# Kernel tuning notes

Hardware: AMD Instinct MI355X
Metric: run time of the kernel (lower is better)

The kernel has to match this reference:

```python
import jax, jax.numpy as jnp
import numpy as np

B, T, E, V, L = 8, 128, 256, 8192, 5  # batch, block_size, embedding_size (== num heads, head_size=1), vocab, num blocks


def setup_inputs() -> dict:
    key = jax.random.key(0)
    ks = jax.random.split(key, 12)
    s = 0.02
    return {
        "idxs": jax.random.randint(ks[0], (B, T), 0, V),
        "targets": jax.random.randint(ks[1], (B, T), 0, V),
        "emb": jax.random.normal(ks[2], (V, E)) * s,
        "pos_emb": jax.random.normal(ks[3], (T, E)) * s,
        "Wq": jax.random.normal(ks[4], (L, E, E)) * s,  # per-layer: E heads, each Linear(E,1); columns are heads
        "Wk": jax.random.normal(ks[5], (L, E, E)) * s,
        "Wv": jax.random.normal(ks[6], (L, E, E)) * s,
        "Wfc": jax.random.normal(ks[7], (L, E, E)) * s,
        "bfc": jnp.zeros((L, E)),
        "Wlm": jax.random.normal(ks[8], (E, V)) * s,
        "blm": jnp.zeros((V,)),
    }


def _block(x, Wq, Wk, Wv, Wfc, bfc):
    # E heads of head_size=1: projecting with [E,E] gives [B,T,H] with H==E,
    # column h being head h's scalar q/k/v. Faithful to per-head Linear(E,1).
    q = x @ Wq
    k = x @ Wk
    v = x @ Wv
    scores = jnp.einsum('bih,bjh->bhij', q, k)  # no 1/sqrt(d) scaling (faithful)
    i = jnp.arange(x.shape[1])
    causal = i[:, None] >= i[None, :]  # masked_fill where tril==0, i.e. j>i -> -inf
    scores = jnp.where(causal[None, None], scores, -jnp.inf)
    attn = jax.nn.softmax(scores, axis=-2)  # NOTE: source softmaxes over dim=-2 (query axis) -- faithful quirk
    out = jnp.einsum('bhij,bjh->bih', attn, v)  # concat of heads == H axis order
    x = x + out
    return x + jax.nn.relu(x @ Wfc + bfc)


def reference(idxs, targets, emb, pos_emb, Wq, Wk, Wv, Wfc, bfc, Wlm, blm):
    x = emb[idxs] + pos_emb[: idxs.shape[1]]  # [B,T,E]
    for l in range(L):
        x = _block(x, Wq[l], Wk[l], Wv[l], Wfc[l], bfc[l])
    logits = (x @ Wlm + blm).reshape(-1, V)  # [B*T, V], as source views before CE
    logp = jax.nn.log_softmax(logits, axis=-1)
    loss = -jnp.take_along_axis(logp, targets.reshape(-1, 1), axis=-1).mean()
    return logits, loss
```

## Files before the change

### kernel.cpp

```cpp
#include <hip/hip_runtime.h>

#define BB 8
#define TT 128
#define EE 256
#define VV 8192
#define LL 5
#define NROWS (BB*TT)

typedef __attribute__((ext_vector_type(8))) short bf16x8;
typedef __attribute__((ext_vector_type(4))) float f32x4;

__device__ inline ushort f2bf(float f) {
    union { float f; unsigned u; } c; c.f = f;
    unsigned u = c.u;
    return (ushort)((u + 0x7FFF + ((u >> 16) & 1)) >> 16);
}

__device__ __forceinline__ void gload_lds16(const void* g, void* l) {
    __builtin_amdgcn_global_load_lds((const __attribute__((address_space(1))) unsigned int*)g,
                                     (__attribute__((address_space(3))) unsigned int*)l,
                                     16, 0, 0);
}


__global__ __launch_bounds__(256) void prep_kernel(
        const int* __restrict__ idxs, const float* __restrict__ emb, const float* __restrict__ pos,
        const float* __restrict__ Wq, const float* __restrict__ Wk,
        const float* __restrict__ Wv, const float* __restrict__ Wfc,
        const float* __restrict__ Wlm,
        float* __restrict__ x0, ushort* __restrict__ WTs, ushort* __restrict__ WlmT,
        float* __restrict__ loss_cell) {
    int id = blockIdx.x;
    if (id == 0) {
        if (threadIdx.x == 0) *loss_cell = 0.f;
        return;
    }
    if (id < 513) {
        __shared__ ushort ts[64][72];
        int idw = id - 1;
        int v0 = (idw & 127) * 64, k0 = (idw >> 7) * 64;
        int lane = threadIdx.x & 63, w = threadIdx.x >> 6;
        for (int kk = w; kk < 64; kk += 4)
            ts[lane][kk] = f2bf(Wlm[(size_t)(k0 + kk)*VV + v0 + lane]);
        __syncthreads();
        for (int vv = w; vv < 64; vv += 4) {
            int r = v0 + vv, k = k0 + lane;
            WlmT[(size_t)r*256 + (k & 128) + ((k & 127) ^ ((r & 7) << 3))] = ts[vv][lane];
        }
        return;
    }
    if (id < 833) {
        __shared__ ushort ts[64][72];
        int idm = id - 513;
        int mat = idm >> 4, tile = idm & 15;
        int l = mat >> 2, type = mat & 3;
        const float* src = (type == 0 ? Wq : type == 1 ? Wk : type == 2 ? Wv : Wfc) + l*EE*EE;
        ushort* dst = WTs + mat*EE*EE;
        int i0 = (tile >> 2) * 64, o0 = (tile & 3) * 64;
        int lane = threadIdx.x & 63, w = threadIdx.x >> 6;
        for (int ii = w; ii < 64; ii += 4)
            ts[lane][ii] = f2bf(src[(i0 + ii)*EE + o0 + lane]);
        __syncthreads();
        for (int oo = w; oo < 64; oo += 4) {
            int r = o0 + oo, k = i0 + lane;
            dst[(size_t)r*256 + (k & 128) + ((k & 127) ^ ((r & 7) << 3))] = ts[oo][lane];
        }
        return;
    }
    int h = threadIdx.x;
    int row0 = (id - 833) * 4;
    for (int r = 0; r < 4; ++r) {
        int row = row0 + r;
        x0[row*EE + h] = emb[(size_t)idxs[row]*EE + h] + pos[(row & (TT-1))*EE + h];
    }
}

__global__ __launch_bounds__(512, 4) void qkv_attn_kernel(
        float* __restrict__ x, const ushort* __restrict__ WTl) {
    __shared__ __align__(16) ushort Xs[128*128];
    __shared__ __align__(16) ushort Bs[32*128];
    __shared__ float QS[8*132], KS[8*132], VS[8*132], MS[8*132], RV[8*132];
    int tid = threadIdx.x, lane = tid & 63, w = tid >> 6;
    int b  = blockIdx.x >> 5;
    int h0 = (blockIdx.x & 31) * 8;

    f32x4 acc[2] = {};
    int rband = w*16 + (lane & 15);
    int kq = (lane >> 4) * 8;

    #pragma unroll
    for (int half = 0; half < 2; ++half) {
        if (half) __syncthreads();
        {
            int rsub = lane >> 5, cb = (lane & 31) * 4;
            for (int rr2 = w*2; rr2 < 128; rr2 += 16) {
                int rr = rr2 + rsub;
                float4 v = *(const float4*)&x[(size_t)(b*TT + rr)*EE + half*128 + cb];
                ushort4 hh; hh.x = f2bf(v.x); hh.y = f2bf(v.y); hh.z = f2bf(v.z); hh.w = f2bf(v.w);
                *(ushort4*)&Xs[rr*128 + (cb ^ ((rr & 7) << 3))] = hh;
            }
        }
        {
            int rowg = w*4 + (lane >> 4);
            int rowv = rowg < 24 ? rowg : 23;
            int mat = rowv >> 3, col = h0 + (rowv & 7);
            const ushort* src = WTl + (size_t)mat*EE*EE + (size_t)col*256
                              + half*128 + (lane & 15)*8;
            gload_lds16(src, &Bs[w*4*128]);
        }
        __syncthreads();
        for (int ks = 0; ks < 4; ++ks) {
            int kk = ks*32 + kq;
            bf16x8 a = *(const bf16x8*)&Xs[rband*128 + (kk ^ ((rband & 7) << 3))];
            #pragma unroll
            for (int ct = 0; ct < 2; ++ct) {
                int c = ct*16 + (lane & 15);
                bf16x8 bb = *(const bf16x8*)&Bs[c*128 + (kk ^ ((c & 7) << 3))];
                acc[ct] = __builtin_amdgcn_mfma_f32_16x16x32_bf16(a, bb, acc[ct], 0, 0, 0);
            }
        }
    }
    {
        int r_ = w*16 + ((lane >> 4) << 2);
        #pragma unroll
        for (int ct = 0; ct < 2; ++ct) {
            int col24 = ct*16 + (lane & 15);
            #pragma unroll
            for (int j = 0; j < 4; ++j) {
                float val = acc[ct][j];
                int row = r_ + j;
                if (col24 < 8)       QS[col24*132 + row] = val;
                else if (col24 < 16) KS[(col24-8)*132 + row] = val;
                else if (col24 < 24) VS[(col24-16)*132 + row] = val;
            }
        }
    }
    __syncthreads();

    int g = w, lg = lane;
    {
        int j0 = lg*2;
        float k0 = KS[g*132 + j0], k1 = KS[g*132 + j0 + 1];
        float q0j = QS[g*132 + j0], q1j = QS[g*132 + j0 + 1];
        float pmax = fmaxf(q0j, q1j), pmin = fminf(q0j, q1j);
        #pragma unroll
        for (int d = 1; d < 64; d <<= 1) {
            float om = __shfl_down(pmax, d);
            float on = __shfl_down(pmin, d);
            if (lg + d < 64) { pmax = fmaxf(pmax, om); pmin = fminf(pmin, on); }
        }
        float nx = __shfl_down(pmax, 1), nn = __shfl_down(pmin, 1);
        float sp1 = (lg == 63) ? q1j : fmaxf(q1j, nx);
        float sn1 = (lg == 63) ? q1j : fminf(q1j, nn);
        float m0 = (k0 >= 0.f) ? k0*pmax : k0*pmin;
        float m1 = (k1 >= 0.f) ? k1*sp1  : k1*sn1;
        float z0 = 0.f, z1 = 0.f;
        for (int i = j0; i < TT; ++i) {
            float qi = QS[g*132 + i];
            z0 += __expf(qi*k0 - m0);
            z1 += (i >= j0+1) ? __expf(qi*k1 - m1) : 0.f;
        }
        MS[g*132 + j0]     = m0;
        MS[g*132 + j0 + 1] = m1;
        RV[g*132 + j0]     = VS[g*132 + j0] / z0;
        RV[g*132 + j0 + 1] = VS[g*132 + j0 + 1] / z1;
    }
    __syncthreads();
    float a0 = 0.f, a1 = 0.f;
    {
        int i0 = lg*2;
        float q0 = QS[g*132 + i0], q1 = QS[g*132 + i0 + 1];
        for (int j = 0; j <= i0 + 1; ++j) {
            float kj = KS[g*132 + j], mj = MS[g*132 + j], rj = RV[g*132 + j];
            float e0 = __expf(q0*kj - mj) * rj;
            float e1 = __expf(q1*kj - mj) * rj;
            a0 += (j <= i0) ? e0 : 0.f;
            a1 += e1;
        }
    }
    __syncthreads();
    VS[g*132 + lg*2]     = a0;
    VS[g*132 + lg*2 + 1] = a1;
    __syncthreads();

    {
        int row = tid >> 2, cp = (tid & 3) * 2;
        size_t gx = (size_t)(b*TT + row)*EE + h0 + cp;
        float2 xv = *(float2*)&x[gx];
        xv.x += VS[cp*132 + row];
        xv.y += VS[(cp+1)*132 + row];
        *(float2*)&x[gx] = xv;
    }
}

__global__ __launch_bounds__(256, 4) void fc_mfma(
        const float* __restrict__ xin, const ushort* __restrict__ WT,
        const float* __restrict__ bfc, float* __restrict__ xout) {
    __shared__ __align__(16) ushort As[64*128];
    __shared__ __align__(16) ushort Bs[64*128];
    int tid = threadIdx.x, lane = tid & 63, w = tid >> 6;
    int c0 = blockIdx.x * 64;
    int r0 = blockIdx.y * 64;

    f32x4 acc[4] = {};
    int rband = w*16 + (lane & 15);
    int kq = (lane >> 4) * 8;

    #pragma unroll
    for (int half = 0; half < 2; ++half) {
        if (half) __syncthreads();
        {
            int rsub = lane >> 5, cb = (lane & 31) * 4;
            for (int rr2 = w*2; rr2 < 64; rr2 += 8) {
                int rr = rr2 + rsub;
                float4 v = *(const float4*)&xin[(size_t)(r0 + rr)*EE + half*128 + cb];
                ushort4 hh; hh.x = f2bf(v.x); hh.y = f2bf(v.y); hh.z = f2bf(v.z); hh.w = f2bf(v.w);
                *(ushort4*)&As[rr*128 + (cb ^ ((rr & 7) << 3))] = hh;
            }
        }
        for (int rg = w*4; rg < 64; rg += 16) {
            int row = c0 + rg + (lane >> 4);
            const ushort* src = WT + (size_t)row*256 + half*128 + (lane & 15)*8;
            gload_lds16(src, &Bs[rg*128]);
        }
        __syncthreads();
        for (int ks = 0; ks < 4; ++ks) {
            int kk = ks*32 + kq;
            bf16x8 a = *(const bf16x8*)&As[rband*128 + (kk ^ ((rband & 7) << 3))];
            #pragma unroll
            for (int n = 0; n < 4; ++n) {
                int c = n*16 + (lane & 15);
                bf16x8 b = *(const bf16x8*)&Bs[c*128 + (kk ^ ((c & 7) << 3))];
                acc[n] = __builtin_amdgcn_mfma_f32_16x16x32_bf16(a, b, acc[n], 0, 0, 0);
            }
        }
    }
    int grow0 = r0 + w*16 + ((lane >> 4) << 2);
    #pragma unroll
    for (int n = 0; n < 4; ++n) {
        int col = c0 + n*16 + (lane & 15);
        float bias = bfc[col];
        #pragma unroll
        for (int j = 0; j < 4; ++j) {
            size_t idx = (size_t)(grow0 + j)*EE + col;
            xout[idx] = xin[idx] + fmaxf(acc[n][j] + bias, 0.f);
        }
    }
}

__global__ __launch_bounds__(512, 4) void lm_mfma_kernel(
        const float* __restrict__ x, const ushort* __restrict__ WlmT,
        const float* __restrict__ blm, float* __restrict__ out,
        float* __restrict__ pm, float* __restrict__ pz) {
    __shared__ __align__(16) char LDSb[128*132*4];
    ushort* As = (ushort*)LDSb;
    ushort* Bs = (ushort*)LDSb + 128*128;
    float*  fst = (float*)LDSb;
    int tid = threadIdx.x;
    int lane = tid & 63, w = tid >> 6;
    int c0 = blockIdx.x * 128;
    int r0 = blockIdx.y * 128;

    int wr = (w >> 2) * 64, wc = (w & 3) * 32;
    f32x4 acc[4][2] = {};
    int kq = (lane >> 4) * 8;

    #pragma unroll
    for (int half = 0; half < 2; ++half) {
        if (half) __syncthreads();
        {
            int rsub = lane >> 5, cb = (lane & 31) * 4;
            for (int rr2 = w*2; rr2 < 128; rr2 += 16) {
                int rr = rr2 + rsub;
                float4 v = *(const float4*)&x[(size_t)(r0 + rr)*EE + half*128 + cb];
                ushort4 hh; hh.x = f2bf(v.x); hh.y = f2bf(v.y); hh.z = f2bf(v.z); hh.w = f2bf(v.w);
                *(ushort4*)&As[rr*128 + (cb ^ ((rr & 7) << 3))] = hh;
            }
        }
        for (int rg = w*4; rg < 128; rg += 32) {
            int row = c0 + rg + (lane >> 4);
            const ushort* src = WlmT + (size_t)row*256 + half*128 + (lane & 15)*8;
            gload_lds16(src, &Bs[rg*128]);
        }
        __syncthreads();
        for (int ks = 0; ks < 4; ++ks) {
            int kk = ks*32 + kq;
            bf16x8 a[4], bfr[2];
            #pragma unroll
            for (int m = 0; m < 4; ++m) {
                int rband = wr + m*16 + (lane & 15);
                a[m] = *(const bf16x8*)&As[rband*128 + (kk ^ ((rband & 7) << 3))];
            }
            #pragma unroll
            for (int n = 0; n < 2; ++n) {
                int c = wc + n*16 + (lane & 15);
                bfr[n] = *(const bf16x8*)&Bs[c*128 + (kk ^ ((c & 7) << 3))];
            }
            #pragma unroll
            for (int m = 0; m < 4; ++m)
                #pragma unroll
                for (int n = 0; n < 2; ++n)
                    acc[m][n] = __builtin_amdgcn_mfma_f32_16x16x32_bf16(a[m], bfr[n], acc[m][n], 0, 0, 0);
        }
    }
    __syncthreads();

    float bias[2];
    #pragma unroll
    for (int n = 0; n < 2; ++n) bias[n] = blm[c0 + wc + n*16 + (lane & 15)];
    #pragma unroll
    for (int m = 0; m < 4; ++m) {
        int rw = wr + m*16 + (lane >> 4)*4;
        #pragma unroll
        for (int j = 0; j < 4; ++j) {
            int row = rw + j;
            float vals[2];
            float vmax = -INFINITY;
            #pragma unroll
            for (int n = 0; n < 2; ++n) {
                vals[n] = acc[m][n][j] + bias[n];
                fst[row*132 + wc + n*16 + (lane & 15)] = vals[n];
                vmax = fmaxf(vmax, vals[n]);
            }
            #pragma unroll
            for (int msk = 1; msk <= 8; msk <<= 1) vmax = fmaxf(vmax, __shfl_xor(vmax, msk));
            float z = 0.f;
            #pragma unroll
            for (int n = 0; n < 2; ++n) z += __expf(vals[n] - vmax);
            #pragma unroll
            for (int msk = 1; msk <= 8; msk <<= 1) z += __shfl_xor(z, msk);
            if ((lane & 15) == 0) {
                pm[(size_t)(r0 + row)*256 + blockIdx.x*4 + (w & 3)] = vmax;
                pz[(size_t)(r0 + row)*256 + blockIdx.x*4 + (w & 3)] = z;
            }
        }
    }
    __syncthreads();
    #pragma unroll
    for (int it = 0; it < 8; ++it) {
        int k = tid + it*512;
        int row = k >> 5, c4 = (k & 31)*4;
        float4 v = *(float4*)&fst[row*132 + c4];
        *(float4*)&out[(size_t)(r0 + row)*VV + c0 + c4] = v;
    }
}

__global__ void loss_kernel(const float* __restrict__ pm, const float* __restrict__ pz,
                            const float* __restrict__ logits, const int* __restrict__ targets,
                            float* __restrict__ out_last) {
    int r = blockIdx.x;
    int t = threadIdx.x;
    __shared__ float sm[256], sz[256];
    float m = pm[(size_t)r*256 + t];
    float z = pz[(size_t)r*256 + t];
    sm[t] = m; __syncthreads();
    for (int s = 128; s > 0; s >>= 1) {
        if (t < s) sm[t] = fmaxf(sm[t], sm[t + s]);
        __syncthreads();
    }
    float M = sm[0];
    sz[t] = z * __expf(m - M); __syncthreads();
    for (int s = 128; s > 0; s >>= 1) {
        if (t < s) sz[t] += sz[t + s];
        __syncthreads();
    }
    if (t == 0) {
        float lse = M + logf(sz[0]);
        atomicAdd(out_last, (lse - logits[(size_t)r*VV + targets[r]]) * (1.0f / NROWS));
    }
}

extern "C" void kernel_launch(void* const* d_in, const int* in_sizes, int n_in,
                              void* d_out, int out_size, void* d_ws, size_t ws_size,
                              hipStream_t stream) {
    const int*   idxs    = (const int*)d_in[0];
    const int*   targets = (const int*)d_in[1];
    const float* emb     = (const float*)d_in[2];
    const float* pos     = (const float*)d_in[3];
    const float* Wq      = (const float*)d_in[4];
    const float* Wk      = (const float*)d_in[5];
    const float* Wv      = (const float*)d_in[6];
    const float* Wfc     = (const float*)d_in[7];
    const float* bfc     = (const float*)d_in[8];
    const float* Wlm     = (const float*)d_in[9];
    const float* blm     = (const float*)d_in[10];
    float* out = (float*)d_out;
    float* loss_cell = out + (size_t)NROWS * VV;

    float* ws = (float*)d_ws;
    float*  xa   = ws;
    float*  xb   = xa + NROWS*EE;
    float*  pm   = xb + NROWS*EE;
    float*  pz   = pm + NROWS*256;
    ushort* WTs  = (ushort*)(pz + NROWS*256);
    ushort* WlmT = WTs + 20*EE*EE;

    prep_kernel<<<1089, 256, 0, stream>>>(idxs, emb, pos, Wq, Wk, Wv, Wfc, Wlm,
                                          xa, WTs, WlmT, loss_cell);

    for (int l = 0; l < LL; ++l) {
        float* xi = (l & 1) ? xb : xa;
        float* xo = (l & 1) ? xa : xb;
        qkv_attn_kernel<<<256, 512, 0, stream>>>(xi, WTs + (size_t)l*4*EE*EE);
        fc_mfma<<<dim3(4, 16), 256, 0, stream>>>(xi, WTs + (size_t)(l*4 + 3)*EE*EE,
                                                 bfc + l*EE, xo);
    }

    lm_mfma_kernel<<<dim3(VV/128, NROWS/128), 512, 0, stream>>>(xb, WlmT, blm, out, pm, pz);
    loss_kernel<<<NROWS, 256, 0, stream>>>(pm, pz, out, targets, loss_cell);
}
```

Measured before the change: 204.2 us.

## Fuse previous layer's FC into next layer's QKV-attention kernel

```diff
diff --git a/kernel.cpp b/kernel.cpp
--- a/kernel.cpp
+++ b/kernel.cpp
@@ -15,6 +15,10 @@
     unsigned u = c.u;
     return (ushort)((u + 0x7FFF + ((u >> 16) & 1)) >> 16);
 }
+__device__ inline float bf2f(ushort u) {
+    union { unsigned u; float f; } c; c.u = ((unsigned)u) << 16;
+    return c.f;
+}
 
 __device__ __forceinline__ void gload_lds16(const void* g, void* l) {
     __builtin_amdgcn_global_load_lds((const __attribute__((address_space(1))) unsigned int*)g,
@@ -24,11 +28,10 @@
 
 
 __global__ __launch_bounds__(256) void prep_kernel(
-        const int* __restrict__ idxs, const float* __restrict__ emb, const float* __restrict__ pos,
         const float* __restrict__ Wq, const float* __restrict__ Wk,
         const float* __restrict__ Wv, const float* __restrict__ Wfc,
         const float* __restrict__ Wlm,
-        float* __restrict__ x0, ushort* __restrict__ WTs, ushort* __restrict__ WlmT,
+        ushort* __restrict__ WTs, ushort* __restrict__ WlmT,
         float* __restrict__ loss_cell) {
     int id = blockIdx.x;
     if (id == 0) {
@@ -49,7 +52,7 @@
         }
         return;
     }
-    if (id < 833) {
+    {
         __shared__ ushort ts[64][72];
         int idm = id - 513;
         int mat = idm >> 4, tile = idm & 15;
@@ -65,61 +68,127 @@
             int r = o0 + oo, k = i0 + lane;
             dst[(size_t)r*256 + (k & 128) + ((k & 127) ^ ((r & 7) << 3))] = ts[oo][lane];
         }
-        return;
-    }
-    int h = threadIdx.x;
-    int row0 = (id - 833) * 4;
-    for (int r = 0; r < 4; ++r) {
-        int row = row0 + r;
-        x0[row*EE + h] = emb[(size_t)idxs[row]*EE + h] + pos[(row & (TT-1))*EE + h];
-    }
-}
-
-__global__ __launch_bounds__(512, 4) void qkv_attn_kernel(
-        float* __restrict__ x, const ushort* __restrict__ WTl) {
-    __shared__ __align__(16) ushort Xs[128*128];
-    __shared__ __align__(16) ushort Bs[32*128];
-    __shared__ float QS[8*132], KS[8*132], VS[8*132], MS[8*132], RV[8*132];
+    }
+}
+
+template<bool FIRST>
+__global__ __launch_bounds__(512, 2) void layer_kernel(
+        const float* __restrict__ y_in, float* __restrict__ y_out,
+        const ushort* __restrict__ WTfc, const float* __restrict__ bfc_prev,
+        const ushort* __restrict__ WTqkv,
+        const int* __restrict__ idxs, const float* __restrict__ emb,
+        const float* __restrict__ pos) {
+    __shared__ __align__(16) ushort Zbuf[128*256];
+    __shared__ __align__(16) char U[49152];
+    __shared__ __align__(16) ushort Bsq[32*128];
+    ushort* Ybuf = (ushort*)U;
+    ushort* BsF  = (ushort*)U + 128*128;
+    float* QS = (float*)U;
+    float* KS = QS + 8*132;
+    float* VS = KS + 8*132;
+    float* MS = VS + 8*132;
+    float* RV = MS + 8*132;
     int tid = threadIdx.x, lane = tid & 63, w = tid >> 6;
     int b  = blockIdx.x >> 5;
     int h0 = (blockIdx.x & 31) * 8;
 
+    if (FIRST) {
+        for (int rr = w; rr < 128; rr += 8) {
+            int id = idxs[b*TT + rr];
+            float4 v = *(const float4*)&emb[(size_t)id*EE + lane*4];
+            float4 p = *(const float4*)&pos[rr*EE + lane*4];
+            ushort4 hh;
+            hh.x = f2bf(v.x + p.x); hh.y = f2bf(v.y + p.y);
+            hh.z = f2bf(v.z + p.z); hh.w = f2bf(v.w + p.w);
+            int k0 = lane*4;
+            *(ushort4*)&Zbuf[rr*256 + (k0 & 128) + ((k0 & 127) ^ ((rr & 7) << 3))] = hh;
+        }
+    } else {
+        f32x4 accz[4][4] = {};
+        int rband = w*16 + (lane & 15);
+        int kq = (lane >> 4) * 8;
+        #pragma unroll
+        for (int half = 0; half < 2; ++half) {
+            __syncthreads();
+            {
+                int rsub = lane >> 5, cb = (lane & 31) * 4;
+                for (int rr2 = w*2; rr2 < 128; rr2 += 16) {
+                    int rr = rr2 + rsub;
+                    float4 v = *(const float4*)&y_in[(size_t)(b*TT + rr)*EE + half*128 + cb];
+                    ushort4 hh;
+                    hh.x = f2bf(v.x); hh.y = f2bf(v.y); hh.z = f2bf(v.z); hh.w = f2bf(v.w);
+                    *(ushort4*)&Ybuf[rr*128 + (cb ^ ((rr & 7) << 3))] = hh;
+                }
+            }
+            #pragma unroll
+            for (int cg = 0; cg < 4; ++cg) {
+                __syncthreads();
+                {
+                    int rg = w*4 + (lane >> 4);
+                    const ushort* s0 = WTfc + (size_t)(cg*64 + rg)*256 + half*128 + (lane & 15)*8;
+                    gload_lds16(s0, &BsF[(size_t)w*4*128]);
+                    const ushort* s1 = WTfc + (size_t)(cg*64 + 32 + rg)*256 + half*128 + (lane & 15)*8;
+                    gload_lds16(s1, &BsF[(size_t)(32 + w*4)*128]);
+                }
+                __syncthreads();
+                for (int ks = 0; ks < 4; ++ks) {
+                    int kk = ks*32 + kq;
+                    bf16x8 a = *(const bf16x8*)&Ybuf[rband*128 + (kk ^ ((rband & 7) << 3))];
+                    #pragma unroll
+                    for (int n = 0; n < 4; ++n) {
+                        int c = n*16 + (lane & 15);
+                        bf16x8 bb = *(const bf16x8*)&BsF[c*128 + (kk ^ ((c & 7) << 3))];
+                        accz[cg][n] = __builtin_amdgcn_mfma_f32_16x16x32_bf16(a, bb, accz[cg][n], 0, 0, 0);
+                    }
+                }
+            }
+        }
+        __syncthreads();
+        int grow0 = w*16 + ((lane >> 4) << 2);
+        #pragma unroll
+        for (int cg = 0; cg < 4; ++cg) {
+            #pragma unroll
+            for (int n = 0; n < 4; ++n) {
+                int col = cg*64 + n*16 + (lane & 15);
+                float bias = bfc_prev[col];
+                #pragma unroll
+                for (int j = 0; j < 4; ++j) {
+                    int row = grow0 + j;
+                    float yv = y_in[(size_t)(b*TT + row)*EE + col];
+                    float z = yv + fmaxf(accz[cg][n][j] + bias, 0.f);
+                    Zbuf[row*256 + (col & 128) + ((col & 127) ^ ((row & 7) << 3))] = f2bf(z);
+                }
+            }
+        }
+    }
+
     f32x4 acc[2] = {};
     int rband = w*16 + (lane & 15);
     int kq = (lane >> 4) * 8;
-
     #pragma unroll
     for (int half = 0; half < 2; ++half) {
-        if (half) __syncthreads();
-        {
-            int rsub = lane >> 5, cb = (lane & 31) * 4;
-            for (int rr2 = w*2; rr2 < 128; rr2 += 16) {
-                int rr = rr2 + rsub;
-                float4 v = *(const float4*)&x[(size_t)(b*TT + rr)*EE + half*128 + cb];
-                ushort4 hh; hh.x = f2bf(v.x); hh.y = f2bf(v.y); hh.z = f2bf(v.z); hh.w = f2bf(v.w);
-                *(ushort4*)&Xs[rr*128 + (cb ^ ((rr & 7) << 3))] = hh;
-            }
-        }
+        __syncthreads();
         {
             int rowg = w*4 + (lane >> 4);
             int rowv = rowg < 24 ? rowg : 23;
             int mat = rowv >> 3, col = h0 + (rowv & 7);
-            const ushort* src = WTl + (size_t)mat*EE*EE + (size_t)col*256
+            const ushort* src = WTqkv + (size_t)mat*EE*EE + (size_t)col*256
                               + half*128 + (lane & 15)*8;
-            gload_lds16(src, &Bs[w*4*128]);
+            gload_lds16(src, &Bsq[(size_t)w*4*128]);
         }
         __syncthreads();
         for (int ks = 0; ks < 4; ++ks) {
             int kk = ks*32 + kq;
-            bf16x8 a = *(const bf16x8*)&Xs[rband*128 + (kk ^ ((rband & 7) << 3))];
+            bf16x8 a = *(const bf16x8*)&Zbuf[rband*256 + half*128 + (kk ^ ((rband & 7) << 3))];
             #pragma unroll
             for (int ct = 0; ct < 2; ++ct) {
                 int c = ct*16 + (lane & 15);
-                bf16x8 bb = *(const bf16x8*)&Bs[c*128 + (kk ^ ((c & 7) << 3))];
+                bf16x8 bb = *(const bf16x8*)&Bsq[c*128 + (kk ^ ((c & 7) << 3))];
                 acc[ct] = __builtin_amdgcn_mfma_f32_16x16x32_bf16(a, bb, acc[ct], 0, 0, 0);
             }
         }
     }
+    __syncthreads();
     {
         int r_ = w*16 + ((lane >> 4) << 2);
         #pragma unroll
@@ -185,11 +254,13 @@
 
     {
         int row = tid >> 2, cp = (tid & 3) * 2;
-        size_t gx = (size_t)(b*TT + row)*EE + h0 + cp;
-        float2 xv = *(float2*)&x[gx];
-        xv.x += VS[cp*132 + row];
-        xv.y += VS[(cp+1)*132 + row];
-        *(float2*)&x[gx] = xv;
+        int c0i = h0 + cp, c1i = h0 + cp + 1;
+        float z0 = bf2f(Zbuf[row*256 + (c0i & 128) + ((c0i & 127) ^ ((row & 7) << 3))]);
+        float z1 = bf2f(Zbuf[row*256 + (c1i & 128) + ((c1i & 127) ^ ((row & 7) << 3))]);
+        float2 ov;
+        ov.x = z0 + VS[cp*132 + row];
+        ov.y = z1 + VS[(cp+1)*132 + row];
+        *(float2*)&y_out[(size_t)(b*TT + row)*EE + h0 + cp] = ov;
     }
 }
 
@@ -221,7 +292,7 @@
         for (int rg = w*4; rg < 64; rg += 16) {
             int row = c0 + rg + (lane >> 4);
             const ushort* src = WT + (size_t)row*256 + half*128 + (lane & 15)*8;
-            gload_lds16(src, &Bs[rg*128]);
+            gload_lds16(src, &Bs[(size_t)rg*128]);
         }
         __syncthreads();
         for (int ks = 0; ks < 4; ++ks) {
@@ -280,7 +351,7 @@
         for (int rg = w*4; rg < 128; rg += 32) {
             int row = c0 + rg + (lane >> 4);
             const ushort* src = WlmT + (size_t)row*256 + half*128 + (lane & 15)*8;
-            gload_lds16(src, &Bs[rg*128]);
+            gload_lds16(src, &Bs[(size_t)rg*128]);
         }
         __syncthreads();
         for (int ks = 0; ks < 4; ++ks) {
@@ -388,24 +459,28 @@
     float* loss_cell = out + (size_t)NROWS * VV;
 
     float* ws = (float*)d_ws;
-    float*  xa   = ws;
-    float*  xb   = xa + NROWS*EE;
-    float*  pm   = xb + NROWS*EE;
+    float*  ya   = ws;
+    float*  yb   = ya + NROWS*EE;
+    float*  pm   = yb + NROWS*EE;
     float*  pz   = pm + NROWS*256;
     ushort* WTs  = (ushort*)(pz + NROWS*256);
     ushort* WlmT = WTs + 20*EE*EE;
 
-    prep_kernel<<<1089, 256, 0, stream>>>(idxs, emb, pos, Wq, Wk, Wv, Wfc, Wlm,
-                                          xa, WTs, WlmT, loss_cell);
-
-    for (int l = 0; l < LL; ++l) {
-        float* xi = (l & 1) ? xb : xa;
-        float* xo = (l & 1) ? xa : xb;
-        qkv_attn_kernel<<<256, 512, 0, stream>>>(xi, WTs + (size_t)l*4*EE*EE);
-        fc_mfma<<<dim3(4, 16), 256, 0, stream>>>(xi, WTs + (size_t)(l*4 + 3)*EE*EE,
-                                                 bfc + l*EE, xo);
-    }
-
-    lm_mfma_kernel<<<dim3(VV/128, NROWS/128), 512, 0, stream>>>(xb, WlmT, blm, out, pm, pz);
+    prep_kernel<<<833, 256, 0, stream>>>(Wq, Wk, Wv, Wfc, Wlm, WTs, WlmT, loss_cell);
+
+    layer_kernel<true><<<256, 512, 0, stream>>>(
+        nullptr, ya, nullptr, nullptr, WTs + 0, idxs, emb, pos);
+    for (int l = 1; l < LL; ++l) {
+        const float* yi = (l & 1) ? ya : yb;
+        float*       yo = (l & 1) ? yb : ya;
+        layer_kernel<false><<<256, 512, 0, stream>>>(
+            yi, yo,
+            WTs + (size_t)((l-1)*4 + 3)*EE*EE, bfc + (size_t)(l-1)*EE,
+            WTs + (size_t)l*4*EE*EE, idxs, emb, pos);
+    }
+    fc_mfma<<<dim3(4, 16), 256, 0, stream>>>(ya, WTs + (size_t)(4*4 + 3)*EE*EE,
+                                             bfc + 4*EE, yb);
+
+    lm_mfma_kernel<<<dim3(VV/128, NROWS/128), 512, 0, stream>>>(yb, WlmT, blm, out, pm, pz);
     loss_kernel<<<NROWS, 256, 0, stream>>>(pm, pz, out, targets, loss_cell);
 }
```

Result: slower. 218.0 us (+6.8%).

## Fuse weight prep and embedding into layer-0 attention kernel

Applied to the files above, without the earlier changes.

```diff
diff --git a/kernel.cpp b/kernel.cpp
--- a/kernel.cpp
+++ b/kernel.cpp
@@ -23,66 +23,58 @@
 }
 
 
-__global__ __launch_bounds__(256) void prep_kernel(
+__global__ __launch_bounds__(512, 2) void layer0_kernel(
         const int* __restrict__ idxs, const float* __restrict__ emb, const float* __restrict__ pos,
         const float* __restrict__ Wq, const float* __restrict__ Wk,
         const float* __restrict__ Wv, const float* __restrict__ Wfc,
         const float* __restrict__ Wlm,
-        float* __restrict__ x0, ushort* __restrict__ WTs, ushort* __restrict__ WlmT,
+        float* __restrict__ y_out, ushort* __restrict__ WTs, ushort* __restrict__ WlmT,
         float* __restrict__ loss_cell) {
-    int id = blockIdx.x;
-    if (id == 0) {
-        if (threadIdx.x == 0) *loss_cell = 0.f;
-        return;
-    }
-    if (id < 513) {
-        __shared__ ushort ts[64][72];
-        int idw = id - 1;
-        int v0 = (idw & 127) * 64, k0 = (idw >> 7) * 64;
-        int lane = threadIdx.x & 63, w = threadIdx.x >> 6;
-        for (int kk = w; kk < 64; kk += 4)
-            ts[lane][kk] = f2bf(Wlm[(size_t)(k0 + kk)*VV + v0 + lane]);
-        __syncthreads();
-        for (int vv = w; vv < 64; vv += 4) {
-            int r = v0 + vv, k = k0 + lane;
-            WlmT[(size_t)r*256 + (k & 128) + ((k & 127) ^ ((r & 7) << 3))] = ts[vv][lane];
-        }
-        return;
-    }
-    if (id < 833) {
-        __shared__ ushort ts[64][72];
-        int idm = id - 513;
-        int mat = idm >> 4, tile = idm & 15;
-        int l = mat >> 2, type = mat & 3;
-        const float* src = (type == 0 ? Wq : type == 1 ? Wk : type == 2 ? Wv : Wfc) + l*EE*EE;
-        ushort* dst = WTs + mat*EE*EE;
-        int i0 = (tile >> 2) * 64, o0 = (tile & 3) * 64;
-        int lane = threadIdx.x & 63, w = threadIdx.x >> 6;
-        for (int ii = w; ii < 64; ii += 4)
-            ts[lane][ii] = f2bf(src[(i0 + ii)*EE + o0 + lane]);
-        __syncthreads();
-        for (int oo = w; oo < 64; oo += 4) {
-            int r = o0 + oo, k = i0 + lane;
-            dst[(size_t)r*256 + (k & 128) + ((k & 127) ^ ((r & 7) << 3))] = ts[oo][lane];
-        }
-        return;
-    }
-    int h = threadIdx.x;
-    int row0 = (id - 833) * 4;
-    for (int r = 0; r < 4; ++r) {
-        int row = row0 + r;
-        x0[row*EE + h] = emb[(size_t)idxs[row]*EE + h] + pos[(row & (TT-1))*EE + h];
-    }
-}
-
-__global__ __launch_bounds__(512, 4) void qkv_attn_kernel(
-        float* __restrict__ x, const ushort* __restrict__ WTl) {
     __shared__ __align__(16) ushort Xs[128*128];
     __shared__ __align__(16) ushort Bs[32*128];
-    __shared__ float QS[8*132], KS[8*132], VS[8*132], MS[8*132], RV[8*132];
+    __shared__ __align__(16) float QS[8*132], KS[8*132], VS[8*132], MS[8*132], RV[8*132];
     int tid = threadIdx.x, lane = tid & 63, w = tid >> 6;
-    int b  = blockIdx.x >> 5;
-    int h0 = (blockIdx.x & 31) * 8;
+    int blk = blockIdx.x;
+
+    if (blk >= 256) {
+        int id = blk - 256;
+        if (id == 0) {
+            if (tid == 0) *loss_cell = 0.f;
+            return;
+        }
+        ushort (*ts)[72] = (ushort(*)[72])Xs;
+        if (id < 513) {
+            int idw = id - 1;
+            int v0 = (idw & 127) * 64, k0 = (idw >> 7) * 64;
+            for (int kk = w; kk < 64; kk += 8)
+                ts[lane][kk] = f2bf(Wlm[(size_t)(k0 + kk)*VV + v0 + lane]);
+            __syncthreads();
+            for (int vv = w; vv < 64; vv += 8) {
+                int r = v0 + vv, k = k0 + lane;
+                WlmT[(size_t)r*256 + (k & 128) + ((k & 127) ^ ((r & 7) << 3))] = ts[vv][lane];
+            }
+            return;
+        }
+        {
+            int idm = id - 513;
+            int mat = idm >> 4, tile = idm & 15;
+            int l = mat >> 2, type = mat & 3;
+            const float* src = (type == 0 ? Wq : type == 1 ? Wk : type == 2 ? Wv : Wfc) + l*EE*EE;
+            ushort* dst = WTs + mat*EE*EE;
+            int i0 = (tile >> 2) * 64, o0 = (tile & 3) * 64;
+            for (int ii = w; ii < 64; ii += 8)
+                ts[lane][ii] = f2bf(src[(i0 + ii)*EE + o0 + lane]);
+            __syncthreads();
+            for (int oo = w; oo < 64; oo += 8) {
+                int r = o0 + oo, k = i0 + lane;
+                dst[(size_t)r*256 + (k & 128) + ((k & 127) ^ ((r & 7) << 3))] = ts[oo][lane];
+            }
+            return;
+        }
+    }
+
+    int b  = blk >> 5;
+    int h0 = (blk & 31) * 8;
 
     f32x4 acc[2] = {};
     int rband = w*16 + (lane & 15);
@@ -95,18 +87,33 @@
             int rsub = lane >> 5, cb = (lane & 31) * 4;
             for (int rr2 = w*2; rr2 < 128; rr2 += 16) {
                 int rr = rr2 + rsub;
-                float4 v = *(const float4*)&x[(size_t)(b*TT + rr)*EE + half*128 + cb];
-                ushort4 hh; hh.x = f2bf(v.x); hh.y = f2bf(v.y); hh.z = f2bf(v.z); hh.w = f2bf(v.w);
+                int id = idxs[b*TT + rr];
+                float4 v = *(const float4*)&emb[(size_t)id*EE + half*128 + cb];
+                float4 p = *(const float4*)&pos[rr*EE + half*128 + cb];
+                ushort4 hh;
+                hh.x = f2bf(v.x + p.x); hh.y = f2bf(v.y + p.y);
+                hh.z = f2bf(v.z + p.z); hh.w = f2bf(v.w + p.w);
                 *(ushort4*)&Xs[rr*128 + (cb ^ ((rr & 7) << 3))] = hh;
             }
         }
         {
-            int rowg = w*4 + (lane >> 4);
-            int rowv = rowg < 24 ? rowg : 23;
-            int mat = rowv >> 3, col = h0 + (rowv & 7);
-            const ushort* src = WTl + (size_t)mat*EE*EE + (size_t)col*256
-                              + half*128 + (lane & 15)*8;
-            gload_lds16(src, &Bs[w*4*128]);
+            int c = tid >> 4;
+            int kb8 = (tid & 15) * 8;
+            ushort tmp[8];
+            if (c < 24) {
+                int mat = c >> 3;
+                int col = h0 + (c & 7);
+                const float* Wm = mat == 0 ? Wq : (mat == 1 ? Wk : Wv);
+                #pragma unroll
+                for (int i = 0; i < 8; ++i)
+                    tmp[i] = f2bf(Wm[(size_t)(half*128 + kb8 + i)*EE + col]);
+            } else {
+                #pragma unroll
+                for (int i = 0; i < 8; ++i) tmp[i] = 0;
+            }
+            ushort* dst = &Bs[c*128 + (kb8 ^ ((c & 7) << 3))];
+            *(ushort4*)dst       = *(ushort4*)&tmp[0];
+            *(ushort4*)(dst + 4) = *(ushort4*)&tmp[4];
         }
         __syncthreads();
         for (int ks = 0; ks < 4; ++ks) {
@@ -185,6 +192,126 @@
 
     {
         int row = tid >> 2, cp = (tid & 3) * 2;
+        int id = idxs[b*TT + row];
+        float2 ev = *(const float2*)&emb[(size_t)id*EE + h0 + cp];
+        float2 pv = *(const float2*)&pos[row*EE + h0 + cp];
+        float2 ov;
+        ov.x = ev.x + pv.x + VS[cp*132 + row];
+        ov.y = ev.y + pv.y + VS[(cp+1)*132 + row];
+        *(float2*)&y_out[(size_t)(b*TT + row)*EE + h0 + cp] = ov;
+    }
+}
+
+__global__ __launch_bounds__(512, 4) void qkv_attn_kernel(
+        float* __restrict__ x, const ushort* __restrict__ WTl) {
+    __shared__ __align__(16) ushort Xs[128*128];
+    __shared__ __align__(16) ushort Bs[32*128];
+    __shared__ __align__(16) float QS[8*132], KS[8*132], VS[8*132], MS[8*132], RV[8*132];
+    int tid = threadIdx.x, lane = tid & 63, w = tid >> 6;
+    int b  = blockIdx.x >> 5;
+    int h0 = (blockIdx.x & 31) * 8;
+
+    f32x4 acc[2] = {};
+    int rband = w*16 + (lane & 15);
+    int kq = (lane >> 4) * 8;
+
+    #pragma unroll
+    for (int half = 0; half < 2; ++half) {
+        if (half) __syncthreads();
+        {
+            int rsub = lane >> 5, cb = (lane & 31) * 4;
+            for (int rr2 = w*2; rr2 < 128; rr2 += 16) {
+                int rr = rr2 + rsub;
+                float4 v = *(const float4*)&x[(size_t)(b*TT + rr)*EE + half*128 + cb];
+                ushort4 hh; hh.x = f2bf(v.x); hh.y = f2bf(v.y); hh.z = f2bf(v.z); hh.w = f2bf(v.w);
+                *(ushort4*)&Xs[rr*128 + (cb ^ ((rr & 7) << 3))] = hh;
+            }
+        }
+        {
+            int rowg = w*4 + (lane >> 4);
+            int rowv = rowg < 24 ? rowg : 23;
+            int mat = rowv >> 3, col = h0 + (rowv & 7);
+            const ushort* src = WTl + (size_t)mat*EE*EE + (size_t)col*256
+                              + half*128 + (lane & 15)*8;
+            gload_lds16(src, &Bs[(size_t)w*4*128]);
+        }
+        __syncthreads();
+        for (int ks = 0; ks < 4; ++ks) {
+            int kk = ks*32 + kq;
+            bf16x8 a = *(const bf16x8*)&Xs[rband*128 + (kk ^ ((rband & 7) << 3))];
+            #pragma unroll
+            for (int ct = 0; ct < 2; ++ct) {
+                int c = ct*16 + (lane & 15);
+                bf16x8 bb = *(const bf16x8*)&Bs[c*128 + (kk ^ ((c & 7) << 3))];
+                acc[ct] = __builtin_amdgcn_mfma_f32_16x16x32_bf16(a, bb, acc[ct], 0, 0, 0);
+            }
+        }
+    }
+    {
+        int r_ = w*16 + ((lane >> 4) << 2);
+        #pragma unroll
+        for (int ct = 0; ct < 2; ++ct) {
+            int col24 = ct*16 + (lane & 15);
+            #pragma unroll
+            for (int j = 0; j < 4; ++j) {
+                float val = acc[ct][j];
+                int row = r_ + j;
+                if (col24 < 8)       QS[col24*132 + row] = val;
+                else if (col24 < 16) KS[(col24-8)*132 + row] = val;
+                else if (col24 < 24) VS[(col24-16)*132 + row] = val;
+            }
+        }
+    }
+    __syncthreads();
+
+    int g = w, lg = lane;
+    {
+        int j0 = lg*2;
+        float k0 = KS[g*132 + j0], k1 = KS[g*132 + j0 + 1];
+        float q0j = QS[g*132 + j0], q1j = QS[g*132 + j0 + 1];
+        float pmax = fmaxf(q0j, q1j), pmin = fminf(q0j, q1j);
+        #pragma unroll
+        for (int d = 1; d < 64; d <<= 1) {
+            float om = __shfl_down(pmax, d);
+            float on = __shfl_down(pmin, d);
+            if (lg + d < 64) { pmax = fmaxf(pmax, om); pmin = fminf(pmin, on); }
+        }
+        float nx = __shfl_down(pmax, 1), nn = __shfl_down(pmin, 1);
+        float sp1 = (lg == 63) ? q1j : fmaxf(q1j, nx);
+        float sn1 = (lg == 63) ? q1j : fminf(q1j, nn);
+        float m0 = (k0 >= 0.f) ? k0*pmax : k0*pmin;
+        float m1 = (k1 >= 0.f) ? k1*sp1  : k1*sn1;
+        float z0 = 0.f, z1 = 0.f;
+        for (int i = j0; i < TT; ++i) {
+            float qi = QS[g*132 + i];
+            z0 += __expf(qi*k0 - m0);
+            z1 += (i >= j0+1) ? __expf(qi*k1 - m1) : 0.f;
+        }
+        MS[g*132 + j0]     = m0;
+        MS[g*132 + j0 + 1] = m1;
+        RV[g*132 + j0]     = VS[g*132 + j0] / z0;
+        RV[g*132 + j0 + 1] = VS[g*132 + j0 + 1] / z1;
+    }
+    __syncthreads();
+    float a0 = 0.f, a1 = 0.f;
+    {
+        int i0 = lg*2;
+        float q0 = QS[g*132 + i0], q1 = QS[g*132 + i0 + 1];
+        for (int j = 0; j <= i0 + 1; ++j) {
+            float kj = KS[g*132 + j], mj = MS[g*132 + j], rj = RV[g*132 + j];
+            float e0 = __expf(q0*kj - mj) * rj;
+            float e1 = __expf(q1*kj - mj) * rj;
+            a0 += (j <= i0) ? e0 : 0.f;
+            a1 += e1;
+        }
+    }
+    __syncthreads();
+    VS[g*132 + lg*2]     = a0;
+    VS[g*132 + lg*2 + 1] = a1;
+    __syncthreads();
+
+    {
+        int row = tid >> 2, cp = (tid & 3) * 2;
         size_t gx = (size_t)(b*TT + row)*EE + h0 + cp;
         float2 xv = *(float2*)&x[gx];
         xv.x += VS[cp*132 + row];
@@ -221,7 +348,7 @@
         for (int rg = w*4; rg < 64; rg += 16) {
             int row = c0 + rg + (lane >> 4);
             const ushort* src = WT + (size_t)row*256 + half*128 + (lane & 15)*8;
-            gload_lds16(src, &Bs[rg*128]);
+            gload_lds16(src, &Bs[(size_t)rg*128]);
         }
         __syncthreads();
         for (int ks = 0; ks < 4; ++ks) {
@@ -280,7 +407,7 @@
         for (int rg = w*4; rg < 128; rg += 32) {
             int row = c0 + rg + (lane >> 4);
             const ushort* src = WlmT + (size_t)row*256 + half*128 + (lane & 15)*8;
-            gload_lds16(src, &Bs[rg*128]);
+            gload_lds16(src, &Bs[(size_t)rg*128]);
         }
         __syncthreads();
         for (int ks = 0; ks < 4; ++ks) {
@@ -388,24 +515,25 @@
     float* loss_cell = out + (size_t)NROWS * VV;
 
     float* ws = (float*)d_ws;
-    float*  xa   = ws;
-    float*  xb   = xa + NROWS*EE;
-    float*  pm   = xb + NROWS*EE;
+    float*  ya   = ws;
+    float*  yb   = ya + NROWS*EE;
+    float*  pm   = yb + NROWS*EE;
     float*  pz   = pm + NROWS*256;
     ushort* WTs  = (ushort*)(pz + NROWS*256);
     ushort* WlmT = WTs + 20*EE*EE;
 
-    prep_kernel<<<1089, 256, 0, stream>>>(idxs, emb, pos, Wq, Wk, Wv, Wfc, Wlm,
-                                          xa, WTs, WlmT, loss_cell);
-
-    for (int l = 0; l < LL; ++l) {
-        float* xi = (l & 1) ? xb : xa;
-        float* xo = (l & 1) ? xa : xb;
+    layer0_kernel<<<1089, 512, 0, stream>>>(idxs, emb, pos, Wq, Wk, Wv, Wfc, Wlm,
+                                            ya, WTs, WlmT, loss_cell);
+    fc_mfma<<<dim3(4, 16), 256, 0, stream>>>(ya, WTs + (size_t)3*EE*EE, bfc, yb);
+
+    for (int l = 1; l < LL; ++l) {
+        float* xi = (l & 1) ? yb : ya;
+        float* xo = (l & 1) ? ya : yb;
         qkv_attn_kernel<<<256, 512, 0, stream>>>(xi, WTs + (size_t)l*4*EE*EE);
         fc_mfma<<<dim3(4, 16), 256, 0, stream>>>(xi, WTs + (size_t)(l*4 + 3)*EE*EE,
-                                                 bfc + l*EE, xo);
-    }
-
-    lm_mfma_kernel<<<dim3(VV/128, NROWS/128), 512, 0, stream>>>(xb, WlmT, blm, out, pm, pz);
+                                                 bfc + (size_t)l*EE, xo);
+    }
+
+    lm_mfma_kernel<<<dim3(VV/128, NROWS/128), 512, 0, stream>>>(yb, WlmT, blm, out, pm, pz);
     loss_kernel<<<NROWS, 256, 0, stream>>>(pm, pz, out, targets, loss_cell);
 }
```

New measurement: 202.4 us. Within noise of the previous version (-0.8%).
